# Kernel optimization log

Hardware: AMD Instinct MI355X
Metric: run time of the kernel (lower is better)

## Reference

```python
import jax, jax.numpy as jnp
import numpy as np

N = 102400       # total nodes (1024 graphs x 100 nodes)
E = 1638400      # edges (avg degree 16)
B = 1024         # graphs; also GRU sequence length (unbatched 2D GRU input)
F_IN, HID, H1 = 4, 16, 6
OUT, FC1, RNN, ACT = 32, 64, 64, 11


def _gat(x, src, dst, W, a_src, a_dst, b, heads, out_dim, concat):
    # PyG GATConv (eval mode, dropout off), add_self_loops=True
    n = x.shape[0]
    loop = jnp.arange(n, dtype=src.dtype)
    s = jnp.concatenate([src, loop])
    d = jnp.concatenate([dst, loop])
    h = (x @ W.T).reshape(n, heads, out_dim)                 # [N,H,F]
    a_s = (h * a_src).sum(-1)                                # [N,H]
    a_d = (h * a_dst).sum(-1)                                # [N,H]
    e = jax.nn.leaky_relu(a_s[s] + a_d[d], 0.2)              # [E',H]
    m = jax.ops.segment_max(e, d, num_segments=n)
    p = jnp.exp(e - m[d])
    alpha = p / jax.ops.segment_sum(p, d, num_segments=n)[d]
    agg = jax.ops.segment_sum(h[s] * alpha[:, :, None], d, num_segments=n)  # [N,H,F]
    agg = agg.reshape(n, heads * out_dim) if concat else agg.mean(axis=1)
    return agg + b


def _gru(xs, wih, whh, bih, bhh):
    # torch nn.GRU, unbatched: xs is [L, FC1], h0 = zeros
    def step(hp, xt):
        gi = xt @ wih.T + bih
        gh = hp @ whh.T + bhh
        ir, iz, i_n = jnp.split(gi, 3)
        hr, hz, h_n = jnp.split(gh, 3)
        r = jax.nn.sigmoid(ir + hr)
        z = jax.nn.sigmoid(iz + hz)
        ng = jnp.tanh(i_n + r * h_n)
        h = (1.0 - z) * ng + z * hp
        return h, h
    _, ys = jax.lax.scan(step, jnp.zeros((RNN,), xs.dtype), xs)
    return ys


def setup_inputs():
    key = jax.random.key(0)
    ks = jax.random.split(key, 16)
    g = lambda i, shape, fan: jax.random.normal(ks[i], shape, jnp.float32) / np.sqrt(fan)
    x = jax.random.normal(ks[0], (N, F_IN), jnp.float32)
    src = jax.random.randint(ks[1], (E,), 0, N)
    dst = jax.random.randint(ks[2], (E,), 0, N)
    dst = jnp.where(dst == src, (dst + 1) % N, dst)  # no pre-existing self-loops
    edge_index = jnp.stack([src, dst]).astype(jnp.int32)
    robot_index = (jnp.arange(B) * (N // B)).astype(jnp.int32)  # ptr[:-1]
    robot_features = jax.random.normal(ks[3], (B, 4), jnp.float32)
    return dict(
        x=x, edge_index=edge_index, robot_index=robot_index, robot_features=robot_features,
        c1_W=g(4, (H1 * HID, F_IN), F_IN), c1_as=g(5, (H1, HID), HID), c1_ad=g(6, (H1, HID), HID),
        c1_b=jnp.zeros((H1 * HID,), jnp.float32),
        c2_W=g(7, (OUT, H1 * HID), H1 * HID), c2_as=g(8, (1, OUT), OUT), c2_ad=g(9, (1, OUT), OUT),
        c2_b=jnp.zeros((OUT,), jnp.float32),
        fc1_W=g(10, (FC1, OUT + 4), OUT + 4), fc1_b=jnp.zeros((FC1,), jnp.float32),
        gru_wih=g(11, (3 * RNN, FC1), FC1), gru_whh=g(12, (3 * RNN, RNN), RNN),
        gru_bih=jnp.zeros((3 * RNN,), jnp.float32), gru_bhh=jnp.zeros((3 * RNN,), jnp.float32),
        fc2_W=g(13, (ACT, RNN), RNN), fc2_b=jnp.zeros((ACT,), jnp.float32),
    )


def reference(x, edge_index, robot_index, robot_features,
              c1_W, c1_as, c1_ad, c1_b, c2_W, c2_as, c2_ad, c2_b,
              fc1_W, fc1_b, gru_wih, gru_whh, gru_bih, gru_bhh, fc2_W, fc2_b):
    src, dst = edge_index[0], edge_index[1]
    h = _gat(x, src, dst, c1_W, c1_as, c1_ad, c1_b, H1, HID, True)   # [N, 96]
    h = jnp.tanh(h)
    h = _gat(h, src, dst, c2_W, c2_as, c2_ad, c2_b, 1, OUT, False)   # [N, 32]
    h = h[robot_index]                                               # [B, 32]
    h = jnp.tanh(jnp.concatenate([h, robot_features], axis=1) @ fc1_W.T + fc1_b)  # [B, 64]
    h = _gru(h, gru_wih, gru_whh, gru_bih, gru_bhh)                  # [B, 64]
    return h @ fc2_W.T + fc2_b                                       # [B, 11] logits
```

## Files before the change

kernel.cpp:

```cpp
#include <hip/hip_runtime.h>

#define S2CAP 24576
#define ECAP  524288

__device__ __forceinline__ float fsig(float x){ return 1.f/(1.f + __expf(-x)); }
__device__ __forceinline__ float ftanh(float a){
  a = fminf(fmaxf(a, -15.f), 15.f);
  float e2 = __expf(2.f*a);
  return (e2 - 1.f)/(e2 + 1.f);
}
__device__ __forceinline__ float attw(float e){
  e = (e > 0.f) ? e : 0.2f*e;
  return __expf(e);
}

__global__ void k_pre(const float* __restrict__ c1W, const float* __restrict__ c1as,
                      const float* __restrict__ c1ad, float* __restrict__ AsAd){
  int t = threadIdx.x;
  if (t >= 48) return;
  int which = t/24, r = t%24, k = r/6, h = r%6;
  const float* av = which ? c1ad : c1as;
  float s = 0.f;
  for (int f = 0; f < 16; ++f) s += c1W[(h*16+f)*4 + k] * av[h*16+f];
  AsAd[which*24 + k*6 + h] = s;
}

__global__ void k_flag(const int* __restrict__ rix, int B, int* __restrict__ sidx,
                       int* __restrict__ nodeof, int* __restrict__ ctrl){
  int i = blockIdx.x*blockDim.x + threadIdx.x;
  if (i == 0) ctrl[0] = B;
  if (i < B){ int r = rix[i]; sidx[r] = i; nodeof[i] = r; }
}

__global__ void k_claim(const int* __restrict__ ei, int E, int B,
                        int* __restrict__ sidx, int* __restrict__ nodeof,
                        int* __restrict__ ctrl){
  int e = blockIdx.x*blockDim.x + threadIdx.x;
  if (e >= E) return;
  int d = ei[E + e];
  int sd = sidx[d];
  if (sd < 0 || sd >= B) return;
  int s = ei[e];
  if (sidx[s] < 0){
    int old = atomicCAS(&sidx[s], -1, -2);
    if (old == -1){
      int id = atomicAdd(&ctrl[0], 1);
      if (id < S2CAP){ nodeof[id] = s; sidx[s] = id; }
      else sidx[s] = -1;
    }
  }
}

__global__ void k_count(const int* __restrict__ ei, int E,
                        const int* __restrict__ sidx, int* __restrict__ cnt1){
  int e = blockIdx.x*blockDim.x + threadIdx.x;
  if (e >= E) return;
  int sd = sidx[ei[E + e]];
  if (sd >= 0) atomicAdd(&cnt1[sd], 1);
}

__global__ void k_scan(const int* __restrict__ cnt, int* __restrict__ off,
                       int* __restrict__ run, int n){
  __shared__ int part[1024];
  int tid = threadIdx.x;
  int per = (n + 1023)/1024;
  int base = tid*per;
  int s = 0;
  for (int i = 0; i < per; ++i){ int idx = base+i; if (idx < n) s += cnt[idx]; }
  part[tid] = s; __syncthreads();
  for (int d = 1; d < 1024; d <<= 1){
    int v = part[tid];
    int o = (tid >= d) ? part[tid-d] : 0;
    __syncthreads();
    part[tid] = v + o;
    __syncthreads();
  }
  int acc = (tid == 0) ? 0 : part[tid-1];
  for (int i = 0; i < per; ++i){
    int idx = base+i;
    if (idx < n){ off[idx] = acc; run[idx] = acc; acc += cnt[idx]; }
  }
}

__global__ void k_scatter(const int* __restrict__ ei, int E,
                          const int* __restrict__ sidx, int* __restrict__ run1,
                          int* __restrict__ csr1){
  int e = blockIdx.x*blockDim.x + threadIdx.x;
  if (e >= E) return;
  int sd = sidx[ei[E + e]];
  if (sd >= 0){
    int p = atomicAdd(&run1[sd], 1);
    if (p < ECAP) csr1[p] = ei[e];
  }
}

__global__ void k_gat1(const float* __restrict__ x, const float* __restrict__ c1W,
                       const float* __restrict__ c1b, const float* __restrict__ AsAd,
                       const int* __restrict__ nodeof, const int* __restrict__ off1,
                       const int* __restrict__ cnt1, const int* __restrict__ csr1,
                       const int* __restrict__ ctrl, float* __restrict__ tbuf){
  int gid = blockIdx.x*blockDim.x + threadIdx.x;
  int sid = gid/6, h = gid - sid*6;
  if (sid >= ctrl[0]) return;
  float Ask[4], Adk[4];
  #pragma unroll
  for (int k = 0; k < 4; ++k){ Ask[k] = AsAd[k*6+h]; Adk[k] = AsAd[24 + k*6 + h]; }
  float W[16][4];
  #pragma unroll
  for (int f = 0; f < 16; ++f)
    #pragma unroll
    for (int k = 0; k < 4; ++k) W[f][k] = c1W[(h*16+f)*4 + k];
  int d = nodeof[sid];
  float4 xd = *(const float4*)(x + 4*(size_t)d);
  float ad = xd.x*Adk[0] + xd.y*Adk[1] + xd.z*Adk[2] + xd.w*Adk[3];
  int beg = off1[sid], n = cnt1[sid];
  if (beg >= ECAP) n = 0; else if (beg + n > ECAP) n = ECAP - beg;
  float den = 0.f, agg[16];
  #pragma unroll
  for (int f = 0; f < 16; ++f) agg[f] = 0.f;
  for (int j = -1; j < n; ++j){
    int s = (j < 0) ? d : csr1[beg + j];
    float4 xv = *(const float4*)(x + 4*(size_t)s);
    float as = xv.x*Ask[0] + xv.y*Ask[1] + xv.z*Ask[2] + xv.w*Ask[3];
    float wgt = attw(as + ad);
    den += wgt;
    #pragma unroll
    for (int f = 0; f < 16; ++f){
      float h1 = xv.x*W[f][0] + xv.y*W[f][1] + xv.z*W[f][2] + xv.w*W[f][3];
      agg[f] = fmaf(wgt, h1, agg[f]);
    }
  }
  float inv = 1.f/den;
  #pragma unroll
  for (int f = 0; f < 16; ++f)
    tbuf[(size_t)sid*96 + h*16 + f] = ftanh(agg[f]*inv + c1b[h*16+f]);
}

__global__ void k_h2(const float* __restrict__ c2W, const float* __restrict__ tbuf,
                     const int* __restrict__ ctrl, float* __restrict__ h2){
  int gid = blockIdx.x*blockDim.x + threadIdx.x;
  int sid = gid >> 5, o = gid & 31;
  if (sid >= ctrl[0]) return;
  const float* t = tbuf + (size_t)sid*96;
  const float* wr = c2W + o*96;
  float s = 0.f;
  #pragma unroll
  for (int j = 0; j < 96; ++j) s = fmaf(wr[j], t[j], s);
  h2[(size_t)sid*32 + o] = s;
}

__global__ void k_att2(const float* __restrict__ h2, const float* __restrict__ c2as,
                       const float* __restrict__ c2ad, const int* __restrict__ ctrl,
                       float* __restrict__ as2, float* __restrict__ ad2){
  int sid = blockIdx.x*blockDim.x + threadIdx.x;
  if (sid >= ctrl[0]) return;
  const float* h = h2 + (size_t)sid*32;
  float a = 0.f, b = 0.f;
  #pragma unroll
  for (int o = 0; o < 32; ++o){ a = fmaf(h[o], c2as[o], a); b = fmaf(h[o], c2ad[o], b); }
  as2[sid] = a; ad2[sid] = b;
}

__global__ void k_gat2fc1(const float* __restrict__ h2, const float* __restrict__ as2,
                          const float* __restrict__ ad2, const float* __restrict__ c2b,
                          const float* __restrict__ rf, const float* __restrict__ fc1W,
                          const float* __restrict__ fc1b, const int* __restrict__ sidx,
                          const int* __restrict__ off1, const int* __restrict__ cnt1,
                          const int* __restrict__ csr1, float* __restrict__ xs, int B){
  int rp = blockIdx.x*blockDim.x + threadIdx.x;
  if (rp >= B) return;
  float ad = ad2[rp];
  float den = 0.f, agg[32];
  #pragma unroll
  for (int o = 0; o < 32; ++o) agg[o] = 0.f;
  int beg = off1[rp], n = cnt1[rp];
  if (beg >= ECAP) n = 0; else if (beg + n > ECAP) n = ECAP - beg;
  for (int j = -1; j < n; ++j){
    int ss;
    if (j < 0) ss = rp;
    else { int s = csr1[beg + j]; ss = sidx[s]; if (ss < 0 || ss >= S2CAP) continue; }
    float wgt = attw(as2[ss] + ad);
    den += wgt;
    const float* hv = h2 + (size_t)ss*32;
    #pragma unroll
    for (int o = 0; o < 32; ++o) agg[o] = fmaf(wgt, hv[o], agg[o]);
  }
  float inv = 1.f/den;
  float cat[36];
  #pragma unroll
  for (int o = 0; o < 32; ++o) cat[o] = agg[o]*inv + c2b[o];
  #pragma unroll
  for (int k = 0; k < 4; ++k) cat[32+k] = rf[rp*4+k];
  for (int o = 0; o < 64; ++o){
    float s = fc1b[o];
    const float* wrow = fc1W + o*36;
    #pragma unroll
    for (int j = 0; j < 36; ++j) s = fmaf(wrow[j], cat[j], s);
    xs[(size_t)rp*64 + o] = ftanh(s);
  }
}

__global__ void k_gi(const float* __restrict__ xs, const float* __restrict__ wih,
                     const float* __restrict__ bih, const float* __restrict__ bhh,
                     float* __restrict__ gi, int B){
  int gid = blockIdx.x*blockDim.x + threadIdx.x;
  if (gid >= B*192) return;
  int t = gid/192, g = gid - t*192;
  const float* xv = xs + (size_t)t*64;
  const float* wr = wih + (size_t)g*64;
  float s = bih[g] + (g < 128 ? bhh[g] : 0.f);
  #pragma unroll
  for (int k = 0; k < 64; ++k) s = fmaf(wr[k], xv[k], s);
  gi[gid] = s;
}

__global__ void k_whhT(const float* __restrict__ whh, float* __restrict__ whhT){
  int gid = blockIdx.x*blockDim.x + threadIdx.x;
  if (gid >= 192*64) return;
  int g = gid >> 6, k = gid & 63;
  whhT[k*192 + g] = whh[g*64 + k];
}

__global__ __launch_bounds__(64, 1) void k_gru(const float* __restrict__ gi,
                       const float* __restrict__ whhT, const float* __restrict__ bhh,
                       float* __restrict__ ys, int B){
  int u = threadIdx.x;
  float wr[64], wz[64], wn[64];
  #pragma unroll
  for (int k = 0; k < 64; ++k){
    wr[k] = whhT[k*192 + u];
    wz[k] = whhT[k*192 + 64 + u];
    wn[k] = whhT[k*192 + 128 + u];
  }
  float bn = bhh[128 + u];
  __shared__ __align__(16) float hs[64];
  float hu = 0.f;
  hs[u] = 0.f;
  __syncthreads();
  float grc = gi[u], gzc = gi[64 + u], gnc = gi[128 + u];
  for (int t = 0; t < B; ++t){
    int tn = (t + 1 < B) ? t + 1 : t;
    float grn = gi[tn*192 + u], gzn = gi[tn*192 + 64 + u], gnn = gi[tn*192 + 128 + u];
    float ar = 0.f, az = 0.f, an = bn;
    #pragma unroll
    for (int c = 0; c < 16; ++c){
      float4 h4 = *(const float4*)(hs + 4*c);
      ar = fmaf(wr[4*c+0], h4.x, ar); az = fmaf(wz[4*c+0], h4.x, az); an = fmaf(wn[4*c+0], h4.x, an);
      ar = fmaf(wr[4*c+1], h4.y, ar); az = fmaf(wz[4*c+1], h4.y, az); an = fmaf(wn[4*c+1], h4.y, an);
      ar = fmaf(wr[4*c+2], h4.z, ar); az = fmaf(wz[4*c+2], h4.z, az); an = fmaf(wn[4*c+2], h4.z, an);
      ar = fmaf(wr[4*c+3], h4.w, ar); az = fmaf(wz[4*c+3], h4.w, az); an = fmaf(wn[4*c+3], h4.w, an);
    }
    float r  = fsig(grc + ar);
    float z  = fsig(gzc + az);
    float ng = ftanh(gnc + r*an);
    hu = (1.f - z)*ng + z*hu;
    ys[(size_t)t*64 + u] = hu;
    __syncthreads();
    hs[u] = hu;
    __syncthreads();
    grc = grn; gzc = gzn; gnc = gnn;
  }
}

__global__ void k_fc2(const float* __restrict__ ys, const float* __restrict__ f2W,
                      const float* __restrict__ f2b, float* __restrict__ out, int B){
  int gid = blockIdx.x*blockDim.x + threadIdx.x;
  if (gid >= B*11) return;
  int t = gid/11, a = gid - t*11;
  const float* hv = ys + (size_t)t*64;
  const float* wr = f2W + a*64;
  float s = f2b[a];
  #pragma unroll
  for (int k = 0; k < 64; ++k) s = fmaf(wr[k], hv[k], s);
  out[gid] = s;
}

extern "C" void kernel_launch(void* const* d_in, const int* in_sizes, int n_in,
                              void* d_out, int out_size, void* d_ws, size_t ws_size,
                              hipStream_t stream) {
  (void)n_in; (void)out_size; (void)ws_size;
  const float* x    = (const float*)d_in[0];
  const int*   ei   = (const int*)d_in[1];
  const int*   rix  = (const int*)d_in[2];
  const float* rf   = (const float*)d_in[3];
  const float* c1W  = (const float*)d_in[4];
  const float* c1as = (const float*)d_in[5];
  const float* c1ad = (const float*)d_in[6];
  const float* c1b  = (const float*)d_in[7];
  const float* c2W  = (const float*)d_in[8];
  const float* c2as = (const float*)d_in[9];
  const float* c2ad = (const float*)d_in[10];
  const float* c2b  = (const float*)d_in[11];
  const float* fc1W = (const float*)d_in[12];
  const float* fc1b = (const float*)d_in[13];
  const float* wih  = (const float*)d_in[14];
  const float* whh  = (const float*)d_in[15];
  const float* bih  = (const float*)d_in[16];
  const float* bhh  = (const float*)d_in[17];
  const float* f2W  = (const float*)d_in[18];
  const float* f2b  = (const float*)d_in[19];
  float* out = (float*)d_out;

  const int N = in_sizes[0]/4;
  const int E = in_sizes[1]/2;
  const int B = in_sizes[2];

  char* w = (char*)d_ws;
  size_t off = 0;
  auto take = [&](size_t bytes)->char*{
    char* p = w + off;
    off = (off + bytes + 255) & ~(size_t)255;
    return p;
  };
  int*   ctrl   = (int*)  take(256);
  float* AsAd   = (float*)take(256);
  int*   sidx   = (int*)  take((size_t)N*4);
  int*   nodeof = (int*)  take((size_t)S2CAP*4);
  int*   cnt1   = (int*)  take((size_t)S2CAP*4);
  int*   off1   = (int*)  take((size_t)S2CAP*4);
  int*   run1   = (int*)  take((size_t)S2CAP*4);
  int*   csr1   = (int*)  take((size_t)ECAP*4);
  float* tbuf   = (float*)take((size_t)S2CAP*96*4);
  float* h2     = (float*)take((size_t)S2CAP*32*4);
  float* as2    = (float*)take((size_t)S2CAP*4);
  float* ad2    = (float*)take((size_t)S2CAP*4);
  float* xs     = (float*)take((size_t)B*64*4);
  float* gi     = (float*)take((size_t)B*192*4);
  float* whhT   = (float*)take((size_t)192*64*4);
  float* ys     = (float*)take((size_t)B*64*4);

  hipMemsetAsync(sidx, 0xFF, (size_t)N*4, stream);
  hipMemsetAsync(cnt1, 0, (size_t)S2CAP*4, stream);
  hipMemsetAsync(ctrl, 0, 256, stream);

  k_pre    <<<1, 64, 0, stream>>>(c1W, c1as, c1ad, AsAd);
  k_flag   <<<(B+255)/256, 256, 0, stream>>>(rix, B, sidx, nodeof, ctrl);
  k_claim  <<<(E+255)/256, 256, 0, stream>>>(ei, E, B, sidx, nodeof, ctrl);
  k_count  <<<(E+255)/256, 256, 0, stream>>>(ei, E, sidx, cnt1);
  k_scan   <<<1, 1024, 0, stream>>>(cnt1, off1, run1, S2CAP);
  k_scatter<<<(E+255)/256, 256, 0, stream>>>(ei, E, sidx, run1, csr1);
  k_gat1   <<<(S2CAP*6+255)/256, 256, 0, stream>>>(x, c1W, c1b, AsAd, nodeof, off1, cnt1, csr1, ctrl, tbuf);
  k_h2     <<<(S2CAP*32+255)/256, 256, 0, stream>>>(c2W, tbuf, ctrl, h2);
  k_att2   <<<(S2CAP+255)/256, 256, 0, stream>>>(h2, c2as, c2ad, ctrl, as2, ad2);
  k_gat2fc1<<<(B+255)/256, 256, 0, stream>>>(h2, as2, ad2, c2b, rf, fc1W, fc1b, sidx, off1, cnt1, csr1, xs, B);
  k_gi     <<<(B*192+255)/256, 256, 0, stream>>>(xs, wih, bih, bhh, gi, B);
  k_whhT   <<<(192*64+255)/256, 256, 0, stream>>>(whh, whhT);
  k_gru    <<<1, 64, 0, stream>>>(gi, whhT, bhh, ys, B);
  k_fc2    <<<(B*11+255)/256, 256, 0, stream>>>(ys, f2W, f2b, out, B);
}
```

Measured before the change: 1.076 ms.

## Broadcast GRU hidden state via readlane and fuse small kernels

The GRU recurrence now broadcasts the hidden state across the single wave with readlane, replacing the shared-memory round trip and the two barriers per step. Each gate gets split accumulators to shorten the dependency chains. Several small kernels and memsets are fused: init with the AsAd precompute and count zeroing, h2 with the attention dot products via a shuffle reduction, and gi with the whh transpose. This cuts per-step synchronisation on the serial 1024-step recurrence and reduces launch count, at the cost of higher register pressure from holding 192 weights per lane.

After: 1.082 ms. Within noise of the previous version (+0.5%).

```diff
diff --git a/kernel.cpp b/kernel.cpp
--- a/kernel.cpp
+++ b/kernel.cpp
@@ -14,22 +14,22 @@
   return __expf(e);
 }
 
-__global__ void k_pre(const float* __restrict__ c1W, const float* __restrict__ c1as,
-                      const float* __restrict__ c1ad, float* __restrict__ AsAd){
-  int t = threadIdx.x;
-  if (t >= 48) return;
-  int which = t/24, r = t%24, k = r/6, h = r%6;
-  const float* av = which ? c1ad : c1as;
-  float s = 0.f;
-  for (int f = 0; f < 16; ++f) s += c1W[(h*16+f)*4 + k] * av[h*16+f];
-  AsAd[which*24 + k*6 + h] = s;
-}
-
-__global__ void k_flag(const int* __restrict__ rix, int B, int* __restrict__ sidx,
-                       int* __restrict__ nodeof, int* __restrict__ ctrl){
-  int i = blockIdx.x*blockDim.x + threadIdx.x;
-  if (i == 0) ctrl[0] = B;
-  if (i < B){ int r = rix[i]; sidx[r] = i; nodeof[i] = r; }
+__global__ void k_init(const float* __restrict__ c1W, const float* __restrict__ c1as,
+                       const float* __restrict__ c1ad, float* __restrict__ AsAd,
+                       const int* __restrict__ rix, int B, int* __restrict__ sidx,
+                       int* __restrict__ nodeof, int* __restrict__ ctrl,
+                       int* __restrict__ cnt1){
+  int gid = blockIdx.x*blockDim.x + threadIdx.x;
+  if (gid == 0) ctrl[0] = B;
+  if (gid < 48){
+    int which = gid/24, r = gid%24, k = r/6, h = r%6;
+    const float* av = which ? c1ad : c1as;
+    float s = 0.f;
+    for (int f = 0; f < 16; ++f) s += c1W[(h*16+f)*4 + k] * av[h*16+f];
+    AsAd[which*24 + k*6 + h] = s;
+  }
+  if (gid < B){ int r = rix[gid]; sidx[r] = gid; nodeof[gid] = r; }
+  if (gid < S2CAP) cnt1[gid] = 0;
 }
 
 __global__ void k_claim(const int* __restrict__ ei, int E, int B,
@@ -136,29 +136,29 @@
     tbuf[(size_t)sid*96 + h*16 + f] = ftanh(agg[f]*inv + c1b[h*16+f]);
 }
 
-__global__ void k_h2(const float* __restrict__ c2W, const float* __restrict__ tbuf,
-                     const int* __restrict__ ctrl, float* __restrict__ h2){
+__global__ void k_h2att(const float* __restrict__ c2W, const float* __restrict__ tbuf,
+                        const float* __restrict__ c2as, const float* __restrict__ c2ad,
+                        const int* __restrict__ ctrl, float* __restrict__ h2,
+                        float* __restrict__ as2, float* __restrict__ ad2){
   int gid = blockIdx.x*blockDim.x + threadIdx.x;
   int sid = gid >> 5, o = gid & 31;
-  if (sid >= ctrl[0]) return;
-  const float* t = tbuf + (size_t)sid*96;
-  const float* wr = c2W + o*96;
+  bool act = sid < ctrl[0];
   float s = 0.f;
-  #pragma unroll
-  for (int j = 0; j < 96; ++j) s = fmaf(wr[j], t[j], s);
-  h2[(size_t)sid*32 + o] = s;
-}
-
-__global__ void k_att2(const float* __restrict__ h2, const float* __restrict__ c2as,
-                       const float* __restrict__ c2ad, const int* __restrict__ ctrl,
-                       float* __restrict__ as2, float* __restrict__ ad2){
-  int sid = blockIdx.x*blockDim.x + threadIdx.x;
-  if (sid >= ctrl[0]) return;
-  const float* h = h2 + (size_t)sid*32;
-  float a = 0.f, b = 0.f;
-  #pragma unroll
-  for (int o = 0; o < 32; ++o){ a = fmaf(h[o], c2as[o], a); b = fmaf(h[o], c2ad[o], b); }
-  as2[sid] = a; ad2[sid] = b;
+  if (act){
+    const float* t = tbuf + (size_t)sid*96;
+    const float* wr = c2W + o*96;
+    #pragma unroll
+    for (int j = 0; j < 96; ++j) s = fmaf(wr[j], t[j], s);
+    h2[(size_t)sid*32 + o] = s;
+  }
+  float a = act ? s*c2as[o] : 0.f;
+  float b = act ? s*c2ad[o] : 0.f;
+  #pragma unroll
+  for (int w = 16; w >= 1; w >>= 1){
+    a += __shfl_xor(a, w, 32);
+    b += __shfl_xor(b, w, 32);
+  }
+  if (act && o == 0){ as2[sid] = a; ad2[sid] = b; }
 }
 
 __global__ void k_gat2fc1(const float* __restrict__ h2, const float* __restrict__ as2,
@@ -200,28 +200,30 @@
   }
 }
 
-__global__ void k_gi(const float* __restrict__ xs, const float* __restrict__ wih,
-                     const float* __restrict__ bih, const float* __restrict__ bhh,
-                     float* __restrict__ gi, int B){
-  int gid = blockIdx.x*blockDim.x + threadIdx.x;
-  if (gid >= B*192) return;
-  int t = gid/192, g = gid - t*192;
-  const float* xv = xs + (size_t)t*64;
-  const float* wr = wih + (size_t)g*64;
-  float s = bih[g] + (g < 128 ? bhh[g] : 0.f);
-  #pragma unroll
-  for (int k = 0; k < 64; ++k) s = fmaf(wr[k], xv[k], s);
-  gi[gid] = s;
-}
-
-__global__ void k_whhT(const float* __restrict__ whh, float* __restrict__ whhT){
-  int gid = blockIdx.x*blockDim.x + threadIdx.x;
-  if (gid >= 192*64) return;
-  int g = gid >> 6, k = gid & 63;
-  whhT[k*192 + g] = whh[g*64 + k];
-}
-
-__global__ __launch_bounds__(64, 1) void k_gru(const float* __restrict__ gi,
+__global__ void k_giT(const float* __restrict__ xs, const float* __restrict__ wih,
+                      const float* __restrict__ bih, const float* __restrict__ bhh,
+                      float* __restrict__ gi, const float* __restrict__ whh,
+                      float* __restrict__ whhT, int B){
+  int gid = blockIdx.x*blockDim.x + threadIdx.x;
+  int NGI = B*192;
+  if (gid < NGI){
+    int t = gid/192, g = gid - t*192;
+    const float* xv = xs + (size_t)t*64;
+    const float* wr = wih + (size_t)g*64;
+    float s = bih[g] + (g < 128 ? bhh[g] : 0.f);
+    #pragma unroll
+    for (int k = 0; k < 64; ++k) s = fmaf(wr[k], xv[k], s);
+    gi[gid] = s;
+  } else {
+    int q = gid - NGI;
+    if (q < 192*64){
+      int g = q >> 6, k = q & 63;
+      whhT[k*192 + g] = whh[g*64 + k];
+    }
+  }
+}
+
+__global__ __launch_bounds__(64) void k_gru(const float* __restrict__ gi,
                        const float* __restrict__ whhT, const float* __restrict__ bhh,
                        float* __restrict__ ys, int B){
   int u = threadIdx.x;
@@ -232,32 +234,33 @@
     wz[k] = whhT[k*192 + 64 + u];
     wn[k] = whhT[k*192 + 128 + u];
   }
+  #pragma unroll
+  for (int k = 0; k < 64; ++k){
+    asm volatile("" : "+v"(wr[k]), "+v"(wz[k]), "+v"(wn[k]));
+  }
   float bn = bhh[128 + u];
-  __shared__ __align__(16) float hs[64];
   float hu = 0.f;
-  hs[u] = 0.f;
-  __syncthreads();
   float grc = gi[u], gzc = gi[64 + u], gnc = gi[128 + u];
   for (int t = 0; t < B; ++t){
     int tn = (t + 1 < B) ? t + 1 : t;
     float grn = gi[tn*192 + u], gzn = gi[tn*192 + 64 + u], gnn = gi[tn*192 + 128 + u];
-    float ar = 0.f, az = 0.f, an = bn;
-    #pragma unroll
-    for (int c = 0; c < 16; ++c){
-      float4 h4 = *(const float4*)(hs + 4*c);
-      ar = fmaf(wr[4*c+0], h4.x, ar); az = fmaf(wz[4*c+0], h4.x, az); an = fmaf(wn[4*c+0], h4.x, an);
-      ar = fmaf(wr[4*c+1], h4.y, ar); az = fmaf(wz[4*c+1], h4.y, az); an = fmaf(wn[4*c+1], h4.y, an);
-      ar = fmaf(wr[4*c+2], h4.z, ar); az = fmaf(wz[4*c+2], h4.z, az); an = fmaf(wn[4*c+2], h4.z, an);
-      ar = fmaf(wr[4*c+3], h4.w, ar); az = fmaf(wz[4*c+3], h4.w, az); an = fmaf(wn[4*c+3], h4.w, an);
+    float ar0 = 0.f, ar1 = 0.f, az0 = 0.f, az1 = 0.f, an0 = bn, an1 = 0.f;
+    #pragma unroll
+    for (int k = 0; k < 64; k += 2){
+      float h0 = __int_as_float(__builtin_amdgcn_readlane(__float_as_int(hu), k));
+      float h1 = __int_as_float(__builtin_amdgcn_readlane(__float_as_int(hu), k + 1));
+      ar0 = fmaf(wr[k],   h0, ar0);
+      az0 = fmaf(wz[k],   h0, az0);
+      an0 = fmaf(wn[k],   h0, an0);
+      ar1 = fmaf(wr[k+1], h1, ar1);
+      az1 = fmaf(wz[k+1], h1, az1);
+      an1 = fmaf(wn[k+1], h1, an1);
     }
-    float r  = fsig(grc + ar);
-    float z  = fsig(gzc + az);
-    float ng = ftanh(gnc + r*an);
+    float r  = fsig(grc + ar0 + ar1);
+    float z  = fsig(gzc + az0 + az1);
+    float ng = ftanh(gnc + r*(an0 + an1));
     hu = (1.f - z)*ng + z*hu;
     ys[(size_t)t*64 + u] = hu;
-    __syncthreads();
-    hs[u] = hu;
-    __syncthreads();
     grc = grn; gzc = gzn; gnc = gnn;
   }
 }
@@ -330,21 +333,16 @@
   float* ys     = (float*)take((size_t)B*64*4);
 
   hipMemsetAsync(sidx, 0xFF, (size_t)N*4, stream);
-  hipMemsetAsync(cnt1, 0, (size_t)S2CAP*4, stream);
-  hipMemsetAsync(ctrl, 0, 256, stream);
-
-  k_pre    <<<1, 64, 0, stream>>>(c1W, c1as, c1ad, AsAd);
-  k_flag   <<<(B+255)/256, 256, 0, stream>>>(rix, B, sidx, nodeof, ctrl);
+
+  k_init   <<<(S2CAP+255)/256, 256, 0, stream>>>(c1W, c1as, c1ad, AsAd, rix, B, sidx, nodeof, ctrl, cnt1);
   k_claim  <<<(E+255)/256, 256, 0, stream>>>(ei, E, B, sidx, nodeof, ctrl);
   k_count  <<<(E+255)/256, 256, 0, stream>>>(ei, E, sidx, cnt1);
   k_scan   <<<1, 1024, 0, stream>>>(cnt1, off1, run1, S2CAP);
   k_scatter<<<(E+255)/256, 256, 0, stream>>>(ei, E, sidx, run1, csr1);
   k_gat1   <<<(S2CAP*6+255)/256, 256, 0, stream>>>(x, c1W, c1b, AsAd, nodeof, off1, cnt1, csr1, ctrl, tbuf);
-  k_h2     <<<(S2CAP*32+255)/256, 256, 0, stream>>>(c2W, tbuf, ctrl, h2);
-  k_att2   <<<(S2CAP+255)/256, 256, 0, stream>>>(h2, c2as, c2ad, ctrl, as2, ad2);
+  k_h2att  <<<(S2CAP*32+255)/256, 256, 0, stream>>>(c2W, tbuf, c2as, c2ad, ctrl, h2, as2, ad2);
   k_gat2fc1<<<(B+255)/256, 256, 0, stream>>>(h2, as2, ad2, c2b, rf, fc1W, fc1b, sidx, off1, cnt1, csr1, xs, B);
-  k_gi     <<<(B*192+255)/256, 256, 0, stream>>>(xs, wih, bih, bhh, gi, B);
-  k_whhT   <<<(192*64+255)/256, 256, 0, stream>>>(whh, whhT);
+  k_giT    <<<(B*192 + 192*64 + 255)/256, 256, 0, stream>>>(xs, wih, bih, bhh, gi, whh, whhT, B);
   k_gru    <<<1, 64, 0, stream>>>(gi, whhT, bhh, ys, B);
   k_fc2    <<<(B*11+255)/256, 256, 0, stream>>>(ys, f2W, f2b, out, B);
 }
```
